# Kernel optimization log

Hardware: AMD Instinct MI355X
Metric: run time of the kernel (lower is better)

Reference implementation:

```python
import jax, jax.numpy as jnp
import numpy as np

# Episode constants (match init_kwargs / input shapes)
B, WAY, SHOT, K = 2, 5, 5, 5
Q_NUM, DIM, HW = 30, 64, 441
BN_EPS = 1e-5


def _episode(q, s, gamma, beta, w3):
    """q: [Q, D, HW] query features; s: [WAY*SHOT, D, HW] support features."""
    # --- cosine logits between mean-pooled query and class prototypes ---
    q_pool = q.mean(axis=2)                                        # [Q, D]
    proto = s.mean(axis=2).reshape(WAY, SHOT, DIM).mean(axis=1)    # [WAY, D]
    qF = q_pool / jnp.linalg.norm(q_pool, axis=-1, keepdims=True)
    pF = proto / jnp.linalg.norm(proto, axis=-1, keepdims=True)
    logits_cos = qF @ pF.T                                         # [Q, WAY]

    # --- spatially L2-normalized descriptors (norm over HW axis, as in torch) ---
    q_norm = q / jnp.linalg.norm(q, axis=2, keepdims=True)         # [Q, D, HW]
    s_norm = s / jnp.linalg.norm(s, axis=2, keepdims=True)         # [WAY*SHOT, D, HW]
    s_l = s_norm.reshape(WAY, SHOT * DIM, HW)                      # [WAY, S*D, HW]
    s_p = jnp.transpose(s_norm, (0, 2, 1)).reshape(WAY, SHOT * HW, DIM)  # [WAY, S*HW, D]

    # channel-level similarity: [Q, WAY, D, SHOT*D], top-k over last axis
    ip_l = jnp.einsum('qdh,wkh->qwdk', q_norm, s_l)
    top_l, _ = jax.lax.top_k(ip_l, K)
    sim_l = top_l.sum(axis=(2, 3))                                 # [Q, WAY]

    # pixel-level similarity: [Q, WAY, HW, SHOT*HW], top-k over last axis
    ip_p = jnp.einsum('qhd,wkd->qwhk', jnp.transpose(q_norm, (0, 2, 1)), s_p)
    top_p, _ = jax.lax.top_k(ip_p, K)
    sim_p = top_p.sum(axis=(2, 3))                                 # [Q, WAY]

    # --- BatchNorm1d(3*WAY), training mode (per-episode batch stats) ---
    feats = jnp.concatenate([logits_cos, sim_l, sim_p], axis=1)    # [Q, 3*WAY]
    mu = feats.mean(axis=0)
    var = feats.var(axis=0)  # biased, as torch BN uses for normalization
    feats_bn = (feats - mu) / jnp.sqrt(var + BN_EPS) * gamma + beta

    # --- Conv1d(1,1,kernel=3,dilation=5,no bias): out length 3*WAY-10 ---
    L = 3 * WAY
    out = w3[0] * feats_bn[:, :L - 10] + w3[1] * feats_bn[:, 5:L - 5] + w3[2] * feats_bn[:, 10:]
    return out                                                      # [Q, WAY]


def setup_inputs() -> dict:
    key = jax.random.key(0)
    k1, k2, k3 = jax.random.split(key, 3)
    return {
        'input1_batch': jax.random.normal(k1, (B * Q_NUM, DIM, HW), dtype=jnp.float32),
        'input2_batch': jax.random.normal(k2, (B * WAY * SHOT, DIM, HW), dtype=jnp.float32),
        'gamma': jnp.ones((3 * WAY,), dtype=jnp.float32),
        'beta': jnp.zeros((3 * WAY,), dtype=jnp.float32),
        'conv_w': jax.random.normal(k3, (1, 1, 3), dtype=jnp.float32),
    }


def reference(input1_batch, input2_batch, gamma, beta, conv_w):
    q = input1_batch.reshape(B, Q_NUM, DIM, HW)
    s = input2_batch.reshape(B, WAY * SHOT, DIM, HW)
    w3 = conv_w.reshape(3)
    sim = jax.vmap(lambda qi, si: _episode(qi, si, gamma, beta, w3))(q, s)
    return sim  # [B, Q_NUM, WAY]
```

## Files before the change

kernel.cpp:

```cpp
#include <hip/hip_runtime.h>
#include <math.h>


typedef __attribute__((ext_vector_type(8))) short bf16x8;
typedef __attribute__((ext_vector_type(4))) float f32x4;

#define MFMA16(a, b, c) __builtin_amdgcn_mfma_f32_16x16x32_bf16((a), (b), (c), 0, 0, 0)

__device__ __forceinline__ unsigned short to_bf16(float v) {
    unsigned int u = __float_as_uint(v);
    unsigned int r = u + 0x7FFFu + ((u >> 16) & 1u);
    return (unsigned short)(r >> 16);
}

__device__ __forceinline__ void ins5(float m[5], float v) {
    m[4] = __builtin_amdgcn_fmed3f(v, m[4], m[3]);
    m[3] = __builtin_amdgcn_fmed3f(v, m[3], m[2]);
    m[2] = __builtin_amdgcn_fmed3f(v, m[2], m[1]);
    m[1] = __builtin_amdgcn_fmed3f(v, m[1], m[0]);
    m[0] = fmaxf(m[0], v);
}

__global__ __launch_bounds__(256) void k1_rownorm(const float* __restrict__ in1,
                                                  const float* __restrict__ in2,
                                                  float* __restrict__ inv_norm,
                                                  float* __restrict__ pool) {
    int wv = threadIdx.x >> 6;
    int lane = threadIdx.x & 63;
    int rid = blockIdx.x * 4 + wv;
    const float* src = (rid < 3840) ? (in1 + (size_t)rid * 441)
                                    : (in2 + (size_t)(rid - 3840) * 441);
    float s = 0.f, ss = 0.f;
#pragma unroll
    for (int i = 0; i < 7; ++i) {
        int h = lane + i * 64;
        if (h < 441) { float v = src[h]; s += v; ss = fmaf(v, v, ss); }
    }
#pragma unroll
    for (int off = 32; off > 0; off >>= 1) {
        s += __shfl_xor(s, off, 64);
        ss += __shfl_xor(ss, off, 64);
    }
    if (lane == 0) {
        inv_norm[rid] = 1.0f / sqrtf(ss);
        pool[rid] = s * (1.0f / 441.0f);
    }
}

__global__ __launch_bounds__(256, 4) void pack_all(const float* __restrict__ in1,
                                                   const float* __restrict__ in2,
                                                   const float* __restrict__ inv_norm,
                                                   const float* __restrict__ pool,
                                                   uint4* __restrict__ Pq,
                                                   uint4* __restrict__ Ps,
                                                   uint4* __restrict__ Al,
                                                   uint4* __restrict__ Bl,
                                                   float* __restrict__ feats) {
    int bid = blockIdx.x;
    int tid = threadIdx.x;
    unsigned short hs[8];
    if (bid < 840) {
        int idx = bid * 256 + tid;
        int lane = idx & 63;
        int ks = (idx >> 6) & 1;
        int rest = idx >> 7;
        int gcs = rest % 840, e = rest / 840;
        int q = gcs / 28, cs = gcs % 28;
        int h = cs * 16 + (lane & 15);
        int d0 = ks * 32 + ((lane >> 4) << 3);
        int rowq = (e * 30 + q) * 64;
#pragma unroll
        for (int j = 0; j < 8; ++j) {
            int d = d0 + j;
            float v = (h < 441) ? in1[(size_t)(rowq + d) * 441 + h] * inv_norm[rowq + d] : 0.f;
            hs[j] = to_bf16(v);
        }
        uint4 H;
        H.x = hs[0] | (hs[1] << 16); H.y = hs[2] | (hs[3] << 16);
        H.z = hs[4] | (hs[5] << 16); H.w = hs[6] | (hs[7] << 16);
        Pq[idx] = H;
    } else if (bid < 1530) {
        int idx = (bid - 840) * 256 + tid;
        int lane = idx & 63;
        int ks = (idx >> 6) & 1;
        int rest = idx >> 7;
        int kt = rest % 138, ew = rest / 138;
        int kidx = kt * 16 + (lane & 15);
        bool valid = kidx < 2205;
        int kc = valid ? kidx : 0;
        int sh = kc / 441;
        int h = kc - sh * 441;
        int e = ew / 5, w = ew % 5;
        int srow = ((e * 25 + w * 5 + sh) * 64);
        int d0 = ks * 32 + ((lane >> 4) << 3);
#pragma unroll
        for (int j = 0; j < 8; ++j) {
            int d = d0 + j;
            float v = valid ? in2[(size_t)(srow + d) * 441 + h] * inv_norm[3840 + srow + d] : 0.f;
            hs[j] = to_bf16(v);
        }
        uint4 H;
        H.x = hs[0] | (hs[1] << 16); H.y = hs[2] | (hs[3] << 16);
        H.z = hs[4] | (hs[5] << 16); H.w = hs[6] | (hs[7] << 16);
        Ps[idx] = H;
    } else if (bid < 2230) {
        int idx = (bid - 1530) * 256 + tid;
        int lane = idx & 63;
        int t2 = idx >> 6;
        int ks = t2 % 14;
        int t3 = t2 / 14;
        int rt = t3 % 20, ew = t3 / 20;
        int e = ew / 5, w = ew % 5;
        int row = rt * 16 + (lane & 15);
        int sh = row >> 6, dp = row & 63;
        int srow = (e * 25 + w * 5 + sh) * 64 + dp;
        int h0 = ks * 32 + ((lane >> 4) << 3);
        const float* src = in2 + (size_t)srow * 441;
        float inv = inv_norm[3840 + srow];
#pragma unroll
        for (int j = 0; j < 8; ++j) {
            int h = h0 + j;
            float v = (h < 441) ? src[h] * inv : 0.f;
            hs[j] = to_bf16(v);
        }
        uint4 H;
        H.x = hs[0] | (hs[1] << 16); H.y = hs[2] | (hs[3] << 16);
        H.z = hs[4] | (hs[5] << 16); H.w = hs[6] | (hs[7] << 16);
        Al[idx] = H;
    } else if (bid < 3070) {
        int idx = (bid - 2230) * 256 + tid;
        int lane = idx & 63;
        int t2 = idx >> 6;
        int ks = t2 % 14;
        int t3 = t2 / 14;
        int gct = t3 % 120, e = t3 / 120;
        int col = gct * 16 + (lane & 15);
        int q = col >> 6, d = col & 63;
        int qrow = (e * 30 + q) * 64 + d;
        int h0 = ks * 32 + ((lane >> 4) << 3);
        const float* src = in1 + (size_t)qrow * 441;
        float inv = inv_norm[qrow];
#pragma unroll
        for (int j = 0; j < 8; ++j) {
            int h = h0 + j;
            float v = (h < 441) ? src[h] * inv : 0.f;
            hs[j] = to_bf16(v);
        }
        uint4 H;
        H.x = hs[0] | (hs[1] << 16); H.y = hs[2] | (hs[3] << 16);
        H.z = hs[4] | (hs[5] << 16); H.w = hs[6] | (hs[7] << 16);
        Bl[idx] = H;
    } else {
        int e = bid - 3070;
        __shared__ float qp[30 * 64], pr[5 * 64], qn[30], pn[5];
        int t = tid;
        for (int li = t; li < 1920; li += 256) qp[li] = pool[e * 30 * 64 + li];
        for (int li = t; li < 320; li += 256) {
            int w = li >> 6, d = li & 63;
            float sm = 0.f;
            for (int sh = 0; sh < 5; ++sh) sm += pool[(60 + e * 25 + w * 5 + sh) * 64 + d];
            pr[li] = sm * 0.2f;
        }
        __syncthreads();
        if (t < 30) {
            float ss = 0.f;
            for (int d = 0; d < 64; ++d) { float v = qp[t * 64 + d]; ss = fmaf(v, v, ss); }
            qn[t] = 1.0f / sqrtf(ss);
        }
        if (t >= 32 && t < 37) {
            int w = t - 32; float ss = 0.f;
            for (int d = 0; d < 64; ++d) { float v = pr[w * 64 + d]; ss = fmaf(v, v, ss); }
            pn[w] = 1.0f / sqrtf(ss);
        }
        __syncthreads();
        if (t < 150) {
            int q = t / 5, w = t % 5;
            float dp = 0.f;
            for (int d = 0; d < 64; ++d) dp = fmaf(qp[q * 64 + d], pr[w * 64 + d], dp);
            feats[(e * 30 + q) * 15 + w] = dp * qn[q] * pn[w];
        }
    }
}

template <int NRR>
__device__ __forceinline__ void chan_pass(int rr0, int ew, int e, int q, int wv, int lane,
                                          const bf16x8* __restrict__ Bl,
                                          const bf16x8* __restrict__ Al,
                                          float m[4][5]) {
    f32x4 cc[NRR][4];
#pragma unroll
    for (int r = 0; r < NRR; ++r)
#pragma unroll
        for (int s = 0; s < 4; ++s) cc[r][s] = (f32x4){0.f, 0.f, 0.f, 0.f};
    for (int ks = 0; ks < 14; ++ks) {
        bf16x8 bh[4];
#pragma unroll
        for (int s = 0; s < 4; ++s)
            bh[s] = Bl[((e * 120 + q * 4 + s) * 14 + ks) * 64 + lane];
#pragma unroll
        for (int r = 0; r < NRR; ++r) {
            bf16x8 ah = Al[((ew * 20 + wv * 5 + rr0 + r) * 14 + ks) * 64 + lane];
#pragma unroll
            for (int s = 0; s < 4; ++s) cc[r][s] = MFMA16(ah, bh[s], cc[r][s]);
        }
    }
#pragma unroll
    for (int r = 0; r < NRR; ++r)
#pragma unroll
        for (int s = 0; s < 4; ++s)
#pragma unroll
            for (int g = 0; g < 4; ++g) ins5(m[s], cc[r][s][g]);
}

__global__ __launch_bounds__(256, 4) void k56(const bf16x8* __restrict__ Pq,
                                              const bf16x8* __restrict__ Ps,
                                              const bf16x8* __restrict__ Bl,
                                              const bf16x8* __restrict__ Al,
                                              float* __restrict__ part_p,
                                              float* __restrict__ siml) {
    __shared__ float Mred[4][64][5];
    int bid = blockIdx.x;
    int tid = threadIdx.x;
    int xcd = bid & 7;
    int slot = bid >> 3;
    int wv = tid >> 6, lane = tid & 63;

    if (slot < 67) {
        int p = xcd * 67 + slot;
        if (p >= 530) return;
        int ew = p / 53;
        int blk = p - ew * 53;
        int e = ew / 5, w = ew - (ew / 5) * 5;
        int gwave = blk * 4 + wv;
        if (gwave >= 210) return;
        int q = gwave / 7;
        int ct0 = gwave * 4;

        bf16x8 Bh[4][2];
#pragma unroll
        for (int s = 0; s < 4; ++s)
#pragma unroll
            for (int ks = 0; ks < 2; ++ks)
                Bh[s][ks] = Pq[((e * 840 + ct0 + s) * 2 + ks) * 64 + lane];

        float m[4][5];
#pragma unroll
        for (int s = 0; s < 4; ++s)
#pragma unroll
            for (int i = 0; i < 5; ++i) m[s][i] = -1e30f;

        int rowbase = (lane >> 4) * 4;

        const bf16x8* As = Ps + (size_t)(ew * 138) * 128 + lane;
        bf16x8 a0 = As[0], a1 = As[64];
        bf16x8 b0 = As[128], b1 = As[192];

        for (int kt = 0; kt < 138; ++kt) {
            bf16x8 n0, n1;
            if (kt < 136) {
                n0 = As[(size_t)(kt + 2) * 128];
                n1 = As[(size_t)(kt + 2) * 128 + 64];
            }
#pragma unroll
            for (int s = 0; s < 4; ++s) {
                f32x4 c = {0.f, 0.f, 0.f, 0.f};
                c = MFMA16(a0, Bh[s][0], c);
                c = MFMA16(a1, Bh[s][1], c);
                if (kt == 137) {
#pragma unroll
                    for (int g = 0; g < 4; ++g) {
                        float v = (rowbase + g < 13) ? c[g] : -1e30f;
                        ins5(m[s], v);
                    }
                } else {
#pragma unroll
                    for (int g = 0; g < 4; ++g) ins5(m[s], c[g]);
                }
            }
            a0 = b0; a1 = b1; b0 = n0; b1 = n1;
        }

#pragma unroll
        for (int mask = 16; mask <= 32; mask <<= 1) {
            float ov[4][5];
#pragma unroll
            for (int s = 0; s < 4; ++s)
#pragma unroll
                for (int i = 0; i < 5; ++i) ov[s][i] = __shfl_xor(m[s][i], mask, 64);
#pragma unroll
            for (int s = 0; s < 4; ++s)
#pragma unroll
                for (int i = 0; i < 5; ++i) ins5(m[s], ov[s][i]);
        }

        float tot = 0.f;
#pragma unroll
        for (int s = 0; s < 4; ++s) {
            float s5 = m[s][0] + m[s][1] + m[s][2] + m[s][3] + m[s][4];
            int h = ((ct0 + s) % 28) * 16 + (lane & 15);
            s5 = (h < 441) ? s5 : 0.f;
#pragma unroll
            for (int mask = 1; mask <= 8; mask <<= 1) s5 += __shfl_xor(s5, mask, 64);
            tot += s5;
        }
        if (lane == 0) {
            int sl = gwave - q * 7;
            part_p[((e * 30 + q) * 5 + w) * 7 + sl] = tot;
        }
    } else {
        int c = xcd * 38 + (slot - 67);
        if (c >= 300) return;
        int ew = c / 30, q = c - ew * 30;
        int e = ew / 5, w = ew - (ew / 5) * 5;

        float m[4][5];
#pragma unroll
        for (int s = 0; s < 4; ++s)
#pragma unroll
            for (int i = 0; i < 5; ++i) m[s][i] = -1e30f;

        chan_pass<3>(0, ew, e, q, wv, lane, Bl, Al, m);
        chan_pass<2>(3, ew, e, q, wv, lane, Bl, Al, m);

#pragma unroll
        for (int mask = 16; mask <= 32; mask <<= 1) {
            float ov[4][5];
#pragma unroll
            for (int s = 0; s < 4; ++s)
#pragma unroll
                for (int i = 0; i < 5; ++i) ov[s][i] = __shfl_xor(m[s][i], mask, 64);
#pragma unroll
            for (int s = 0; s < 4; ++s)
#pragma unroll
                for (int i = 0; i < 5; ++i) ins5(m[s], ov[s][i]);
        }

        if (lane < 16) {
#pragma unroll
            for (int s = 0; s < 4; ++s)
#pragma unroll
                for (int i = 0; i < 5; ++i) Mred[wv][s * 16 + lane][i] = m[s][i];
        }
        __syncthreads();

        if (tid < 64) {
            float lst[5];
#pragma unroll
            for (int i = 0; i < 5; ++i) lst[i] = Mred[0][tid][i];
#pragma unroll
            for (int v2 = 1; v2 < 4; ++v2)
#pragma unroll
                for (int i = 0; i < 5; ++i) ins5(lst, Mred[v2][tid][i]);
            float s5 = lst[0] + lst[1] + lst[2] + lst[3] + lst[4];
#pragma unroll
            for (int mask = 1; mask <= 32; mask <<= 1) s5 += __shfl_xor(s5, mask, 64);
            if (tid == 0) siml[(e * 30 + q) * 5 + w] = s5;
        }
    }
}

__global__ __launch_bounds__(256) void k7_final(const float* __restrict__ feats,
                                                const float* __restrict__ siml,
                                                const float* __restrict__ part_p,
                                                const float* __restrict__ gamma,
                                                const float* __restrict__ beta,
                                                const float* __restrict__ convw,
                                                float* __restrict__ out) {
    int e = blockIdx.x;
    __shared__ float f[30 * 15], mu[15], inv[15];
    int t = threadIdx.x;
    if (t < 150) {
        int q = t / 5, w = t % 5;
        int pb = ((e * 30 + q) * 5 + w) * 7;
        float sp = 0.f;
#pragma unroll
        for (int s = 0; s < 7; ++s) sp += part_p[pb + s];
        f[q * 15 + w] = feats[(e * 30 + q) * 15 + w];
        f[q * 15 + 5 + w] = siml[(e * 30 + q) * 5 + w];
        f[q * 15 + 10 + w] = sp;
    }
    __syncthreads();
    if (t < 15) {
        float s1 = 0.f;
        for (int q = 0; q < 30; ++q) s1 += f[q * 15 + t];
        float mn = s1 * (1.0f / 30.0f);
        float s2 = 0.f;
        for (int q = 0; q < 30; ++q) { float d = f[q * 15 + t] - mn; s2 = fmaf(d, d, s2); }
        mu[t] = mn;
        inv[t] = 1.0f / sqrtf(s2 * (1.0f / 30.0f) + 1e-5f);
    }
    __syncthreads();
    if (t < 150) {
        int q = t / 5, j = t % 5;
        float w0 = convw[0], w1 = convw[1], w2 = convw[2];
        float b0 = (f[q * 15 + j]      - mu[j])      * inv[j]      * gamma[j]      + beta[j];
        float b1 = (f[q * 15 + 5 + j]  - mu[5 + j])  * inv[5 + j]  * gamma[5 + j]  + beta[5 + j];
        float b2 = (f[q * 15 + 10 + j] - mu[10 + j]) * inv[10 + j] * gamma[10 + j] + beta[10 + j];
        out[e * 150 + q * 5 + j] = w0 * b0 + w1 * b1 + w2 * b2;
    }
}

extern "C" void kernel_launch(void* const* d_in, const int* in_sizes, int n_in,
                              void* d_out, int out_size, void* d_ws, size_t ws_size,
                              hipStream_t stream) {
    const float* in1 = (const float*)d_in[0];
    const float* in2 = (const float*)d_in[1];
    const float* gamma = (const float*)d_in[2];
    const float* beta = (const float*)d_in[3];
    const float* convw = (const float*)d_in[4];
    float* out = (float*)d_out;

    char* ws = (char*)d_ws;
    float* inv_norm = (float*)(ws + 0);
    float* pool     = (float*)(ws + 28160);
    float* feats    = (float*)(ws + 56320);
    float* siml     = (float*)(ws + 59920);
    float* part_p   = (float*)(ws + 61120);
    size_t o = 69520;
    uint4* Pq = (uint4*)(ws + o); o += 3440640;
    uint4* Ps = (uint4*)(ws + o); o += 2826240;
    uint4* Al = (uint4*)(ws + o); o += 2867200;
    uint4* Bl = (uint4*)(ws + o); o += 3440640;

    k1_rownorm<<<dim3(1760), dim3(256), 0, stream>>>(in1, in2, inv_norm, pool);
    pack_all<<<dim3(3072), dim3(256), 0, stream>>>(in1, in2, inv_norm, pool,
                                                   Pq, Ps, Al, Bl, feats);
    k56<<<dim3(840), dim3(256), 0, stream>>>((const bf16x8*)Pq, (const bf16x8*)Ps,
                                             (const bf16x8*)Bl, (const bf16x8*)Al,
                                             part_p, siml);
    k7_final<<<dim3(2), dim3(256), 0, stream>>>(feats, siml, part_p, gamma, beta, convw, out);
}
```

Before: 131.8 us.

## Stage support pixel tiles through shared memory with block-cooperative double buffering

In the pixel-similarity branch, the four waves of a block used to each stream the same support tile from global memory on their own. Now the block loads each chunk cooperatively into a double-buffered LDS buffer, syncs, and all waves read their MFMA operands from it. Inactive tail waves stay alive so they still reach the barriers. This cuts redundant global and L2 traffic, at the cost of a block-wide barrier every chunk and larger LDS use, which may limit occupancy.

```diff
diff --git a/kernel.cpp b/kernel.cpp
--- a/kernel.cpp
+++ b/kernel.cpp
@@ -213,17 +213,18 @@
 }
 
 __global__ __launch_bounds__(256, 4) void k56(const bf16x8* __restrict__ Pq,
-                                              const bf16x8* __restrict__ Ps,
+                                              const uint4* __restrict__ PsU4,
                                               const bf16x8* __restrict__ Bl,
                                               const bf16x8* __restrict__ Al,
                                               float* __restrict__ part_p,
                                               float* __restrict__ siml) {
-    __shared__ float Mred[4][64][5];
+    __shared__ uint4 SB[1024];
     int bid = blockIdx.x;
     int tid = threadIdx.x;
     int xcd = bid & 7;
     int slot = bid >> 3;
     int wv = tid >> 6, lane = tid & 63;
+    const f32x4 ZV = {0.f, 0.f, 0.f, 0.f};
 
     if (slot < 67) {
         int p = xcd * 67 + slot;
@@ -232,16 +233,17 @@
         int blk = p - ew * 53;
         int e = ew / 5, w = ew - (ew / 5) * 5;
         int gwave = blk * 4 + wv;
-        if (gwave >= 210) return;
-        int q = gwave / 7;
-        int ct0 = gwave * 4;
+        bool act = gwave < 210;
+        int gv = act ? gwave : 209;
+        int q = gv / 7;
+        int ct0 = gv * 4;
 
         bf16x8 Bh[4][2];
 #pragma unroll
         for (int s = 0; s < 4; ++s)
 #pragma unroll
             for (int ks = 0; ks < 2; ++ks)
-                Bh[s][ks] = Pq[((e * 840 + ct0 + s) * 2 + ks) * 64 + lane];
+                Bh[s][ks] = ((const bf16x8*)Pq)[((e * 840 + ct0 + s) * 2 + ks) * 64 + lane];
 
         float m[4][5];
 #pragma unroll
@@ -250,64 +252,94 @@
             for (int i = 0; i < 5; ++i) m[s][i] = -1e30f;
 
         int rowbase = (lane >> 4) * 4;
-
-        const bf16x8* As = Ps + (size_t)(ew * 138) * 128 + lane;
-        bf16x8 a0 = As[0], a1 = As[64];
-        bf16x8 b0 = As[128], b1 = As[192];
-
-        for (int kt = 0; kt < 138; ++kt) {
-            bf16x8 n0, n1;
-            if (kt < 136) {
-                n0 = As[(size_t)(kt + 2) * 128];
-                n1 = As[(size_t)(kt + 2) * 128 + 64];
-            }
-#pragma unroll
-            for (int s = 0; s < 4; ++s) {
-                f32x4 c = {0.f, 0.f, 0.f, 0.f};
-                c = MFMA16(a0, Bh[s][0], c);
-                c = MFMA16(a1, Bh[s][1], c);
-                if (kt == 137) {
-#pragma unroll
-                    for (int g = 0; g < 4; ++g) {
-                        float v = (rowbase + g < 13) ? c[g] : -1e30f;
+        const uint4* g = PsU4 + (size_t)ew * 138 * 128;
+        const bf16x8* SBf = (const bf16x8*)SB;
+
+        {
+            uint4 r0 = g[tid], r1 = g[tid + 256];
+            SB[tid] = r0; SB[tid + 256] = r1;
+        }
+        __syncthreads();
+
+        for (int c = 0; c < 34; ++c) {
+            uint4 r0 = g[(size_t)(c + 1) * 512 + tid];
+            uint4 r1 = g[(size_t)(c + 1) * 512 + 256 + tid];
+            int rb = (c & 1) * 512;
+            if (act) {
+#pragma unroll
+                for (int j = 0; j < 4; ++j) {
+                    bf16x8 a0 = SBf[rb + j * 128 + lane];
+                    bf16x8 a1 = SBf[rb + j * 128 + 64 + lane];
+#pragma unroll
+                    for (int s = 0; s < 4; ++s) {
+                        f32x4 cv = MFMA16(a0, Bh[s][0], ZV);
+                        cv = MFMA16(a1, Bh[s][1], cv);
+#pragma unroll
+                        for (int gg = 0; gg < 4; ++gg) ins5(m[s], cv[gg]);
+                    }
+                }
+            }
+            int wb = ((c + 1) & 1) * 512;
+            SB[wb + tid] = r0; SB[wb + 256 + tid] = r1;
+            __syncthreads();
+        }
+        if (act) {
+            {
+                bf16x8 a0 = SBf[0 * 128 + lane];
+                bf16x8 a1 = SBf[0 * 128 + 64 + lane];
+#pragma unroll
+                for (int s = 0; s < 4; ++s) {
+                    f32x4 cv = MFMA16(a0, Bh[s][0], ZV);
+                    cv = MFMA16(a1, Bh[s][1], cv);
+#pragma unroll
+                    for (int gg = 0; gg < 4; ++gg) ins5(m[s], cv[gg]);
+                }
+            }
+            {
+                bf16x8 a0 = SBf[1 * 128 + lane];
+                bf16x8 a1 = SBf[1 * 128 + 64 + lane];
+#pragma unroll
+                for (int s = 0; s < 4; ++s) {
+                    f32x4 cv = MFMA16(a0, Bh[s][0], ZV);
+                    cv = MFMA16(a1, Bh[s][1], cv);
+#pragma unroll
+                    for (int gg = 0; gg < 4; ++gg) {
+                        float v = (rowbase + gg < 13) ? cv[gg] : -1e30f;
                         ins5(m[s], v);
                     }
-                } else {
-#pragma unroll
-                    for (int g = 0; g < 4; ++g) ins5(m[s], c[g]);
                 }
             }
-            a0 = b0; a1 = b1; b0 = n0; b1 = n1;
-        }
-
-#pragma unroll
-        for (int mask = 16; mask <= 32; mask <<= 1) {
-            float ov[4][5];
-#pragma unroll
-            for (int s = 0; s < 4; ++s)
-#pragma unroll
-                for (int i = 0; i < 5; ++i) ov[s][i] = __shfl_xor(m[s][i], mask, 64);
-#pragma unroll
-            for (int s = 0; s < 4; ++s)
-#pragma unroll
-                for (int i = 0; i < 5; ++i) ins5(m[s], ov[s][i]);
-        }
-
-        float tot = 0.f;
-#pragma unroll
-        for (int s = 0; s < 4; ++s) {
-            float s5 = m[s][0] + m[s][1] + m[s][2] + m[s][3] + m[s][4];
-            int h = ((ct0 + s) % 28) * 16 + (lane & 15);
-            s5 = (h < 441) ? s5 : 0.f;
-#pragma unroll
-            for (int mask = 1; mask <= 8; mask <<= 1) s5 += __shfl_xor(s5, mask, 64);
-            tot += s5;
-        }
-        if (lane == 0) {
-            int sl = gwave - q * 7;
-            part_p[((e * 30 + q) * 5 + w) * 7 + sl] = tot;
+
+#pragma unroll
+            for (int mask = 16; mask <= 32; mask <<= 1) {
+                float ov[4][5];
+#pragma unroll
+                for (int s = 0; s < 4; ++s)
+#pragma unroll
+                    for (int i = 0; i < 5; ++i) ov[s][i] = __shfl_xor(m[s][i], mask, 64);
+#pragma unroll
+                for (int s = 0; s < 4; ++s)
+#pragma unroll
+                    for (int i = 0; i < 5; ++i) ins5(m[s], ov[s][i]);
+            }
+
+            float tot = 0.f;
+#pragma unroll
+            for (int s = 0; s < 4; ++s) {
+                float s5 = m[s][0] + m[s][1] + m[s][2] + m[s][3] + m[s][4];
+                int h = ((ct0 + s) % 28) * 16 + (lane & 15);
+                s5 = (h < 441) ? s5 : 0.f;
+#pragma unroll
+                for (int mask = 1; mask <= 8; mask <<= 1) s5 += __shfl_xor(s5, mask, 64);
+                tot += s5;
+            }
+            if (lane == 0) {
+                int sl = gv - q * 7;
+                part_p[((e * 30 + q) * 5 + w) * 7 + sl] = tot;
+            }
         }
     } else {
+        float (*Mred)[64][5] = (float (*)[64][5])SB;
         int c = xcd * 38 + (slot - 67);
         if (c >= 300) return;
         int ew = c / 30, q = c - ew * 30;
@@ -425,7 +457,7 @@
     k1_rownorm<<<dim3(1760), dim3(256), 0, stream>>>(in1, in2, inv_norm, pool);
     pack_all<<<dim3(3072), dim3(256), 0, stream>>>(in1, in2, inv_norm, pool,
                                                    Pq, Ps, Al, Bl, feats);
-    k56<<<dim3(840), dim3(256), 0, stream>>>((const bf16x8*)Pq, (const bf16x8*)Ps,
+    k56<<<dim3(840), dim3(256), 0, stream>>>((const bf16x8*)Pq, Ps,
                                              (const bf16x8*)Bl, (const bf16x8*)Al,
                                              part_p, siml);
     k7_final<<<dim3(2), dim3(256), 0, stream>>>(feats, siml, part_p, gamma, beta, convw, out);
```

Result: faster. 128.0 us (median of 2 runs) (-2.9%).

## Split pixel-level K loop across waves with LDS top-5 merge

Applied to the files above, without the earlier changes.

Each pixel-similarity block now handles a single column group, and its four waves split the 138 K-tiles among themselves instead of each wave walking all of them. The per-wave top-5 lists are merged through shared memory by wave 0. The grid grows from 840 to 2408 blocks, and the launch-bounds occupancy hint drops from 4 to 2 blocks per CU. The goal is more parallelism and a shorter serial MFMA/top-k chain per wave. The cost is extra blocks, a __syncthreads-based merge, redundant B-operand loads per wave, and a prefetch pipeline shortened from two tiles to one.

```diff
diff --git a/kernel.cpp b/kernel.cpp
--- a/kernel.cpp
+++ b/kernel.cpp
@@ -212,29 +212,30 @@
             for (int g = 0; g < 4; ++g) ins5(m[s], cc[r][s][g]);
 }
 
-__global__ __launch_bounds__(256, 4) void k56(const bf16x8* __restrict__ Pq,
+__global__ __launch_bounds__(256, 2) void k56(const bf16x8* __restrict__ Pq,
                                               const bf16x8* __restrict__ Ps,
                                               const bf16x8* __restrict__ Bl,
                                               const bf16x8* __restrict__ Al,
                                               float* __restrict__ part_p,
                                               float* __restrict__ siml) {
-    __shared__ float Mred[4][64][5];
+    __shared__ float SH[1280];
     int bid = blockIdx.x;
     int tid = threadIdx.x;
     int xcd = bid & 7;
     int slot = bid >> 3;
     int wv = tid >> 6, lane = tid & 63;
-
-    if (slot < 67) {
-        int p = xcd * 67 + slot;
-        if (p >= 530) return;
-        int ew = p / 53;
-        int blk = p - ew * 53;
+    const f32x4 ZV = {0.f, 0.f, 0.f, 0.f};
+
+    if (slot < 263) {
+        int p = xcd * 263 + slot;
+        if (p >= 2100) return;
+        int ew = p / 210;
+        int gwave = p - ew * 210;
         int e = ew / 5, w = ew - (ew / 5) * 5;
-        int gwave = blk * 4 + wv;
-        if (gwave >= 210) return;
         int q = gwave / 7;
         int ct0 = gwave * 4;
+        int k0 = wv * 35;
+        int kend = (wv == 3) ? 138 : k0 + 35;
 
         bf16x8 Bh[4][2];
 #pragma unroll
@@ -250,34 +251,30 @@
             for (int i = 0; i < 5; ++i) m[s][i] = -1e30f;
 
         int rowbase = (lane >> 4) * 4;
-
         const bf16x8* As = Ps + (size_t)(ew * 138) * 128 + lane;
-        bf16x8 a0 = As[0], a1 = As[64];
-        bf16x8 b0 = As[128], b1 = As[192];
-
-        for (int kt = 0; kt < 138; ++kt) {
-            bf16x8 n0, n1;
-            if (kt < 136) {
-                n0 = As[(size_t)(kt + 2) * 128];
-                n1 = As[(size_t)(kt + 2) * 128 + 64];
-            }
+
+        bf16x8 a0 = As[(size_t)k0 * 128];
+        bf16x8 a1 = As[(size_t)k0 * 128 + 64];
+        for (int kt = k0; kt < kend; ++kt) {
+            int ktn = (kt + 1 < kend) ? kt + 1 : kt;
+            bf16x8 n0 = As[(size_t)ktn * 128];
+            bf16x8 n1 = As[(size_t)ktn * 128 + 64];
 #pragma unroll
             for (int s = 0; s < 4; ++s) {
-                f32x4 c = {0.f, 0.f, 0.f, 0.f};
-                c = MFMA16(a0, Bh[s][0], c);
-                c = MFMA16(a1, Bh[s][1], c);
+                f32x4 cv = MFMA16(a0, Bh[s][0], ZV);
+                cv = MFMA16(a1, Bh[s][1], cv);
                 if (kt == 137) {
 #pragma unroll
-                    for (int g = 0; g < 4; ++g) {
-                        float v = (rowbase + g < 13) ? c[g] : -1e30f;
+                    for (int gg = 0; gg < 4; ++gg) {
+                        float v = (rowbase + gg < 13) ? cv[gg] : -1e30f;
                         ins5(m[s], v);
                     }
                 } else {
 #pragma unroll
-                    for (int g = 0; g < 4; ++g) ins5(m[s], c[g]);
+                    for (int gg = 0; gg < 4; ++gg) ins5(m[s], cv[gg]);
                 }
             }
-            a0 = b0; a1 = b1; b0 = n0; b1 = n1;
+            a0 = n0; a1 = n1;
         }
 
 #pragma unroll
@@ -293,22 +290,36 @@
                 for (int i = 0; i < 5; ++i) ins5(m[s], ov[s][i]);
         }
 
-        float tot = 0.f;
-#pragma unroll
-        for (int s = 0; s < 4; ++s) {
-            float s5 = m[s][0] + m[s][1] + m[s][2] + m[s][3] + m[s][4];
-            int h = ((ct0 + s) % 28) * 16 + (lane & 15);
+        float (*Msh)[4][16][5] = (float (*)[4][16][5])SH;
+        if (lane < 16) {
+#pragma unroll
+            for (int s = 0; s < 4; ++s)
+#pragma unroll
+                for (int i = 0; i < 5; ++i) Msh[wv][s][lane][i] = m[s][i];
+        }
+        __syncthreads();
+        if (wv == 0) {
+            int s = lane >> 4, col = lane & 15;
+            float lst[5];
+#pragma unroll
+            for (int i = 0; i < 5; ++i) lst[i] = Msh[0][s][col][i];
+#pragma unroll
+            for (int w2 = 1; w2 < 4; ++w2)
+#pragma unroll
+                for (int i = 0; i < 5; ++i) ins5(lst, Msh[w2][s][col][i]);
+            float s5 = lst[0] + lst[1] + lst[2] + lst[3] + lst[4];
+            int h = ((ct0 + s) % 28) * 16 + col;
             s5 = (h < 441) ? s5 : 0.f;
 #pragma unroll
-            for (int mask = 1; mask <= 8; mask <<= 1) s5 += __shfl_xor(s5, mask, 64);
-            tot += s5;
-        }
-        if (lane == 0) {
-            int sl = gwave - q * 7;
-            part_p[((e * 30 + q) * 5 + w) * 7 + sl] = tot;
+            for (int mask = 1; mask <= 32; mask <<= 1) s5 += __shfl_xor(s5, mask, 64);
+            if (lane == 0) {
+                int sl = gwave - q * 7;
+                part_p[((e * 30 + q) * 5 + w) * 7 + sl] = s5;
+            }
         }
     } else {
-        int c = xcd * 38 + (slot - 67);
+        float (*Mred)[64][5] = (float (*)[64][5])SH;
+        int c = xcd * 38 + (slot - 263);
         if (c >= 300) return;
         int ew = c / 30, q = c - ew * 30;
         int e = ew / 5, w = ew - (ew / 5) * 5;
@@ -425,8 +436,8 @@
     k1_rownorm<<<dim3(1760), dim3(256), 0, stream>>>(in1, in2, inv_norm, pool);
     pack_all<<<dim3(3072), dim3(256), 0, stream>>>(in1, in2, inv_norm, pool,
                                                    Pq, Ps, Al, Bl, feats);
-    k56<<<dim3(840), dim3(256), 0, stream>>>((const bf16x8*)Pq, (const bf16x8*)Ps,
-                                             (const bf16x8*)Bl, (const bf16x8*)Al,
-                                             part_p, siml);
+    k56<<<dim3(2408), dim3(256), 0, stream>>>((const bf16x8*)Pq, (const bf16x8*)Ps,
+                                              (const bf16x8*)Bl, (const bf16x8*)Al,
+                                              part_p, siml);
     k7_final<<<dim3(2), dim3(256), 0, stream>>>(feats, siml, part_p, gamma, beta, convw, out);
 }
```

After: 131.0 us. About the same (-0.6%).
